# Kernel optimization log

Measured on AMD Instinct MI355X. Metric: run time of the kernel, lower is better.

Reference implementation:

```python
import jax, jax.numpy as jnp
import numpy as np
import math

B, T, D = 2, 2048, 1024
H, HS = 16, 64  # n_heads, head_size; D == H*HS


def setup_inputs() -> dict:
    key = jax.random.key(0)
    k1, k2, k3 = jax.random.split(key, 3)
    x = jax.random.normal(k1, (B, T, D), dtype=jnp.float32)
    w_qkv = jax.random.normal(k2, (D, 3 * D), dtype=jnp.float32) * (1.0 / math.sqrt(D))
    b_qkv = jnp.zeros((3 * D,), dtype=jnp.float32)
    w_out = jax.random.normal(k3, (D, D), dtype=jnp.float32) * (1.0 / math.sqrt(D))
    b_out = jnp.zeros((D,), dtype=jnp.float32)
    return {"x": x, "w_qkv": w_qkv, "b_qkv": b_qkv, "w_out": w_out, "b_out": b_out}


def reference(x, w_qkv, b_qkv, w_out, b_out):
    b, t, d = x.shape
    qkv = x @ w_qkv + b_qkv                       # (B,T,3D)
    q, k, v = jnp.split(qkv, 3, axis=-1)
    # (B,T,D) -> (B,H,T,HS)
    q = q.reshape(b, t, H, HS).transpose(0, 2, 1, 3)
    k = k.reshape(b, t, H, HS).transpose(0, 2, 1, 3)
    v = v.reshape(b, t, H, HS).transpose(0, 2, 1, 3)
    scale = 1.0 / math.sqrt(HS)
    attn = jnp.einsum('bhqd,bhkd->bhqk', q, k) * scale  # (B,H,T,T)
    causal = jnp.tril(jnp.ones((t, t), dtype=bool))
    attn = jnp.where(causal[None, None], attn, -jnp.inf)
    attn = jax.nn.softmax(attn, axis=-1)
    o = jnp.einsum('bhqk,bhkd->bhqd', attn, v)          # (B,H,T,HS)
    o = o.transpose(0, 2, 1, 3).reshape(b, t, d)
    return o @ w_out + b_out
```

## Files before the change

### kernel.cpp

```cpp
#include <hip/hip_runtime.h>
#include <math.h>

#define B_  2
#define T_  2048
#define D_  1024
#define H_  16
#define HS_ 64
#define M_  (B_*T_)

typedef __bf16 bf16x8 __attribute__((ext_vector_type(8)));
typedef float  f32x4  __attribute__((ext_vector_type(4)));
typedef unsigned short u16;

static __device__ __forceinline__ u16 f2bf(float f) {
    __bf16 h = (__bf16)f;
    return *reinterpret_cast<u16*>(&h);
}

static __device__ __forceinline__ void glds16(const u16* g, u16* l) {
    __builtin_amdgcn_global_load_lds(
        (const __attribute__((address_space(1))) void*)g,
        (__attribute__((address_space(3))) void*)l, 16, 0, 0);
}

__global__ __launch_bounds__(256) void prep_kernel(
    const float* __restrict__ x, const float* __restrict__ w_qkv,
    const float* __restrict__ w_out,
    u16* __restrict__ Xb, u16* __restrict__ WqkvT, u16* __restrict__ WoutT)
{
    int bid = blockIdx.x;
    if (bid < 4096) {
        int i = (bid * 256 + threadIdx.x) * 4;
        float4 v = *reinterpret_cast<const float4*>(x + i);
        ushort4 o;
        o.x = f2bf(v.x); o.y = f2bf(v.y); o.z = f2bf(v.z); o.w = f2bf(v.w);
        *reinterpret_cast<ushort4*>(Xb + i) = o;
        return;
    }
    const float* in; u16* out; int C; int c0, r0;
    if (bid < 4096 + 3072) {
        int t = bid - 4096;
        in = w_qkv; out = WqkvT; C = 3 * D_;
        c0 = (t % 96) * 32; r0 = (t / 96) * 32;
    } else {
        int t = bid - 7168;
        in = w_out; out = WoutT; C = D_;
        c0 = (t & 31) * 32; r0 = (t >> 5) * 32;
    }
    __shared__ float tile[32][33];
    int tr = threadIdx.x >> 3, tc4 = (threadIdx.x & 7) * 4;
    float4 v = *reinterpret_cast<const float4*>(in + (size_t)(r0 + tr) * C + c0 + tc4);
    tile[tr][tc4+0] = v.x; tile[tr][tc4+1] = v.y;
    tile[tr][tc4+2] = v.z; tile[tr][tc4+3] = v.w;
    __syncthreads();
    ushort4 o;
    o.x = f2bf(tile[tc4+0][tr]); o.y = f2bf(tile[tc4+1][tr]);
    o.z = f2bf(tile[tc4+2][tr]); o.w = f2bf(tile[tc4+3][tr]);
    *reinterpret_cast<ushort4*>(out + (size_t)(c0 + tr) * D_ + r0 + tc4) = o;
}

template<int MODE, int BM, int BN, int WM, int WN, int NTH>
__global__ __launch_bounds__(NTH, 2) void gemm_bt2(
    const u16* __restrict__ A, const u16* __restrict__ Bt,
    const float* __restrict__ bias,
    float* __restrict__ Cf,
    u16* __restrict__ Qb, u16* __restrict__ Kb, u16* __restrict__ Vt,
    int M, int N, int K)
{
    constexpr int MF  = BM / WM / 16;
    constexpr int NF  = BN / WN / 16;
    constexpr int NLA = BM * 8 / NTH;
    constexpr int NLB = BN * 8 / NTH;

    __shared__ u16 As[2][BM * 64];
    __shared__ u16 Bs[2][BN * 64];

    const int tid  = threadIdx.x;
    const int lane = tid & 63, wave = tid >> 6;
    const int wm = wave / WN, wn = wave % WN;
    const int quad = lane >> 4, lr = lane & 15, x7 = lane & 7;
    const int bm = blockIdx.x, bn = blockIdx.y;

    const u16* Ab = A  + (size_t)(bm * BM) * K;
    const u16* Bb = Bt + (size_t)(bn * BN) * K;

    const u16* srcA[NLA]; int dA[NLA];
    const u16* srcB[NLB]; int dB[NLB];
    #pragma unroll
    for (int j = 0; j < NLA; ++j) {
        int ci = j * NTH + tid, r = ci >> 3, c = (ci & 7) ^ (r & 7);
        srcA[j] = Ab + (size_t)r * K + c * 8;
        dA[j] = ci * 8;
    }
    #pragma unroll
    for (int j = 0; j < NLB; ++j) {
        int ci = j * NTH + tid, r = ci >> 3, c = (ci & 7) ^ (r & 7);
        srcB[j] = Bb + (size_t)r * K + c * 8;
        dB[j] = ci * 8;
    }

    const int eA0 = (wm*(BM/WM) + lr)*64 + ((quad    ) ^ x7)*8;
    const int eA1 = (wm*(BM/WM) + lr)*64 + ((quad | 4) ^ x7)*8;
    const int eB0 = (wn*(BN/WN) + lr)*64 + ((quad    ) ^ x7)*8;
    const int eB1 = (wn*(BN/WN) + lr)*64 + ((quad | 4) ^ x7)*8;

    f32x4 acc[MF][NF] = {};
    const int NT = K >> 6;

    #pragma unroll
    for (int j = 0; j < NLA; ++j) glds16(srcA[j], &As[0][dA[j]]);
    #pragma unroll
    for (int j = 0; j < NLB; ++j) glds16(srcB[j], &Bs[0][dB[j]]);
    #pragma unroll
    for (int j = 0; j < NLA; ++j) glds16(srcA[j] + 64, &As[1][dA[j]]);
    #pragma unroll
    for (int j = 0; j < NLB; ++j) glds16(srcB[j] + 64, &Bs[1][dB[j]]);
    asm volatile("s_waitcnt vmcnt(8)" ::: "memory");
    __builtin_amdgcn_s_barrier();

    for (int t = 0; t < NT; ++t) {
        const u16* Ac = As[t & 1];
        const u16* Bc = Bs[t & 1];
        bf16x8 a[MF], b[NF];

        #pragma unroll
        for (int i = 0; i < MF; ++i)
            a[i] = *reinterpret_cast<const bf16x8*>(Ac + eA0 + i*1024);
        #pragma unroll
        for (int j = 0; j < NF; ++j)
            b[j] = *reinterpret_cast<const bf16x8*>(Bc + eB0 + j*1024);
        __builtin_amdgcn_s_setprio(1);
        #pragma unroll
        for (int i = 0; i < MF; ++i)
            #pragma unroll
            for (int j = 0; j < NF; ++j)
                acc[i][j] = __builtin_amdgcn_mfma_f32_16x16x32_bf16(a[i], b[j], acc[i][j], 0, 0, 0);
        __builtin_amdgcn_s_setprio(0);

        #pragma unroll
        for (int i = 0; i < MF; ++i)
            a[i] = *reinterpret_cast<const bf16x8*>(Ac + eA1 + i*1024);
        #pragma unroll
        for (int j = 0; j < NF; ++j)
            b[j] = *reinterpret_cast<const bf16x8*>(Bc + eB1 + j*1024);
        asm volatile("s_waitcnt lgkmcnt(0)" ::: "memory");
        __builtin_amdgcn_s_barrier();

        if (t + 2 < NT) {
            const int k0 = (t + 2) << 6;
            u16* Ad = As[t & 1]; u16* Bd = Bs[t & 1];
            #pragma unroll
            for (int j = 0; j < NLA; ++j) glds16(srcA[j] + k0, Ad + dA[j]);
            #pragma unroll
            for (int j = 0; j < NLB; ++j) glds16(srcB[j] + k0, Bd + dB[j]);
        }

        __builtin_amdgcn_s_setprio(1);
        #pragma unroll
        for (int i = 0; i < MF; ++i)
            #pragma unroll
            for (int j = 0; j < NF; ++j)
                acc[i][j] = __builtin_amdgcn_mfma_f32_16x16x32_bf16(a[i], b[j], acc[i][j], 0, 0, 0);
        __builtin_amdgcn_s_setprio(0);

        if (t + 2 < NT) { asm volatile("s_waitcnt vmcnt(8)" ::: "memory"); }
        else           { asm volatile("s_waitcnt vmcnt(0)" ::: "memory"); }
        __builtin_amdgcn_s_barrier();
    }

    #pragma unroll
    for (int i = 0; i < MF; ++i) {
        int m0 = bm*BM + wm*(BM/WM) + i*16 + quad*4;
        #pragma unroll
        for (int j = 0; j < NF; ++j) {
            int ncol = bn*BN + wn*(BN/WN) + j*16 + lr;
            float bv = bias[ncol];
            float v4[4];
            #pragma unroll
            for (int r = 0; r < 4; ++r) v4[r] = acc[i][j][r] + bv;
            if (MODE == 1) {
                #pragma unroll
                for (int r = 0; r < 4; ++r)
                    Cf[(size_t)(m0 + r) * N + ncol] = v4[r];
            } else {
                int bb = m0 >> 11, t0 = m0 & (T_ - 1);
                int s = ncol >> 10, rem = ncol & 1023;
                int h = rem >> 6, d = rem & 63;
                int bh = bb * H_ + h;
                if (s == 0) {
                    #pragma unroll
                    for (int r = 0; r < 4; ++r)
                        Qb[((size_t)bh*T_ + t0 + r)*HS_ + d] = f2bf(v4[r] * 0.1803368801111244f);
                } else if (s == 1) {
                    #pragma unroll
                    for (int r = 0; r < 4; ++r)
                        Kb[((size_t)bh*T_ + t0 + r)*HS_ + d] = f2bf(v4[r]);
                } else {
                    ushort4 o;
                    o.x = f2bf(v4[0]); o.y = f2bf(v4[1]);
                    o.z = f2bf(v4[2]); o.w = f2bf(v4[3]);
                    *reinterpret_cast<ushort4*>(&Vt[((size_t)bh*HS_ + d)*T_ + t0]) = o;
                }
            }
        }
    }
}

__global__ __launch_bounds__(256) void attn_kernel(
    const u16* __restrict__ Qb, const u16* __restrict__ Kb,
    const u16* __restrict__ Vt, u16* __restrict__ Ob)
{
    __shared__ u16 Ks[64 * 64];
    __shared__ u16 Vs[64 * 64];
    __shared__ u16 Ps[4][16 * 64];

    int tid  = threadIdx.x;
    int lane = tid & 63, wave = tid >> 6;
    int quad = lane >> 4, lr = lane & 15;

    int lin = blockIdx.x;
    int bh  = (lin & 7) + 8 * ((lin >> 3) & 3);
    int idx = lin >> 5;
    int qt  = idx < 16 ? idx : 47 - idx;
    int qw  = qt * 64 + wave * 16;

    const u16* Qp = Qb + ((size_t)bh * T_ + qw) * HS_;
    bf16x8 qf[2];
    #pragma unroll
    for (int h2 = 0; h2 < 2; ++h2)
        qf[h2] = *reinterpret_cast<const bf16x8*>(Qp + lr*HS_ + h2*32 + quad*8);

    f32x4 Oa[4] = {};
    float lrow[4] = {0.f, 0.f, 0.f, 0.f};

    int e      = quad ^ (lr & 7);
    int rb0    = (lr * 8 + e) * 8;
    int rb1    = (lr * 8 + (e ^ 4)) * 8;
    int offw[4][4];
    #pragma unroll
    for (int nt = 0; nt < 4; ++nt)
        #pragma unroll
        for (int r = 0; r < 4; ++r) {
            int prow = quad*4 + r;
            offw[nt][r] = (prow*8 + ((nt*2 + (lr >> 3)) ^ (prow & 7)))*8 + (lr & 7);
        }
    u16* Psw = Ps[wave];

    int srow = tid >> 3;
    int scol = ((tid & 7) ^ (srow & 7)) * 8;
    const u16* kp0 = Kb + ((size_t)bh*T_ + srow     )*HS_ + scol;
    const u16* kp1 = Kb + ((size_t)bh*T_ + srow + 32)*HS_ + scol;
    const u16* vp0 = Vt + ((size_t)bh*HS_ + srow     )*T_ + scol;
    const u16* vp1 = Vt + ((size_t)bh*HS_ + srow + 32)*T_ + scol;

    bf16x8 kpre0 = *reinterpret_cast<const bf16x8*>(kp0);
    bf16x8 kpre1 = *reinterpret_cast<const bf16x8*>(kp1);
    bf16x8 vpre0 = *reinterpret_cast<const bf16x8*>(vp0);
    bf16x8 vpre1 = *reinterpret_cast<const bf16x8*>(vp1);

    for (int jt = 0; jt <= qt; ++jt) {
        __syncthreads();
        reinterpret_cast<bf16x8*>(Ks)[tid]       = kpre0;
        reinterpret_cast<bf16x8*>(Ks)[tid + 256] = kpre1;
        reinterpret_cast<bf16x8*>(Vs)[tid]       = vpre0;
        reinterpret_cast<bf16x8*>(Vs)[tid + 256] = vpre1;
        if (jt < qt) {
            kp0 += 64*HS_; kp1 += 64*HS_; vp0 += 64; vp1 += 64;
            kpre0 = *reinterpret_cast<const bf16x8*>(kp0);
            kpre1 = *reinterpret_cast<const bf16x8*>(kp1);
            vpre0 = *reinterpret_cast<const bf16x8*>(vp0);
            vpre1 = *reinterpret_cast<const bf16x8*>(vp1);
        }
        __syncthreads();

        f32x4 Sa[4] = {};
        #pragma unroll
        for (int nt = 0; nt < 4; ++nt) {
            bf16x8 bk0 = *reinterpret_cast<const bf16x8*>(Ks + rb0 + nt*1024);
            bf16x8 bk1 = *reinterpret_cast<const bf16x8*>(Ks + rb1 + nt*1024);
            Sa[nt] = __builtin_amdgcn_mfma_f32_16x16x32_bf16(qf[0], bk0, Sa[nt], 0, 0, 0);
            Sa[nt] = __builtin_amdgcn_mfma_f32_16x16x32_bf16(qf[1], bk1, Sa[nt], 0, 0, 0);
        }

        if (jt == qt) {
            int kb = jt * 64;
            #pragma unroll
            for (int nt = 0; nt < 4; ++nt)
                #pragma unroll
                for (int r = 0; r < 4; ++r) {
                    int kg = kb + nt*16 + lr;
                    int qg = qw + quad*4 + r;
                    if (kg > qg) Sa[nt][r] = -INFINITY;
                }
        }

        #pragma unroll
        for (int nt = 0; nt < 4; ++nt)
            #pragma unroll
            for (int r = 0; r < 4; ++r) {
                float pv = __builtin_amdgcn_exp2f(Sa[nt][r]);
                lrow[r] += pv;
                Psw[offw[nt][r]] = f2bf(pv);
            }

        #pragma unroll
        for (int kk = 0; kk < 2; ++kk) {
            int rb = kk ? rb1 : rb0;
            bf16x8 pa = *reinterpret_cast<const bf16x8*>(Psw + rb);
            #pragma unroll
            for (int nt = 0; nt < 4; ++nt) {
                bf16x8 vb = *reinterpret_cast<const bf16x8*>(Vs + rb + nt*1024);
                Oa[nt] = __builtin_amdgcn_mfma_f32_16x16x32_bf16(pa, vb, Oa[nt], 0, 0, 0);
            }
        }
    }

    int b = bh >> 4, h = bh & 15;
    #pragma unroll
    for (int r = 0; r < 4; ++r) {
        float s = lrow[r];
        #pragma unroll
        for (int off = 8; off >= 1; off >>= 1)
            s += __shfl_xor(s, off, 64);
        float inv = 1.f / s;
        int qg = qw + quad*4 + r;
        #pragma unroll
        for (int nt = 0; nt < 4; ++nt) {
            int d = nt*16 + lr;
            Ob[((size_t)b*T_ + qg)*D_ + h*HS_ + d] = f2bf(Oa[nt][r] * inv);
        }
    }
}

extern "C" void kernel_launch(void* const* d_in, const int* in_sizes, int n_in,
                              void* d_out, int out_size, void* d_ws, size_t ws_size,
                              hipStream_t stream) {
    (void)in_sizes; (void)n_in; (void)out_size; (void)ws_size;
    const float* x     = (const float*)d_in[0];
    const float* w_qkv = (const float*)d_in[1];
    const float* b_qkv = (const float*)d_in[2];
    const float* w_out = (const float*)d_in[3];
    const float* b_out = (const float*)d_in[4];
    float* out = (float*)d_out;

    char* ws = (char*)d_ws;
    u16* Xb    = (u16*)ws; ws += (size_t)M_ * D_ * 2;
    u16* WqkvT = (u16*)ws; ws += (size_t)3 * D_ * D_ * 2;
    u16* WoutT = (u16*)ws; ws += (size_t)D_ * D_ * 2;
    u16* Qb    = (u16*)ws; ws += (size_t)M_ * D_ * 2;
    u16* Kb    = (u16*)ws; ws += (size_t)M_ * D_ * 2;
    u16* Vt    = (u16*)ws; ws += (size_t)M_ * D_ * 2;
    u16* Ob    = (u16*)ws; ws += (size_t)M_ * D_ * 2;

    prep_kernel<<<8192, 256, 0, stream>>>(x, w_qkv, w_out, Xb, WqkvT, WoutT);
    gemm_bt2<0, 256, 256, 2, 4, 512><<<dim3(M_/256, 3*D_/256), 512, 0, stream>>>(
        Xb, WqkvT, b_qkv, nullptr, Qb, Kb, Vt, M_, 3*D_, D_);
    attn_kernel<<<1024, 256, 0, stream>>>(Qb, Kb, Vt, Ob);
    gemm_bt2<1, 128, 128, 2, 2, 256><<<dim3(M_/128, D_/128), 256, 0, stream>>>(
        Ob, WoutT, b_out, out, nullptr, nullptr, nullptr, M_, D_, D_);
}
```

Before: 175.7 us.

## Add dedicated QKV GEMM kernel with split-K-half staging and interleaved MFMA pipeline

Replaces the templated GEMM for the QKV projection with a specialized kernel that splits each 64-wide K tile into two 32-wide halves held in separate XOR-swizzled LDS buffers. Global-to-LDS loads for the next tile are issued in four pieces between MFMA quarter-blocks, with barriers and waitcnt placed to overlap memory with compute. The aim is to hide load latency and cut LDS bank conflicts. The cost is many more barriers per iteration and more complex synchronization. The generic GEMM is reduced to the output-projection mode only.

```diff
diff --git a/kernel.cpp b/kernel.cpp
--- a/kernel.cpp
+++ b/kernel.cpp
@@ -59,12 +59,149 @@
     *reinterpret_cast<ushort4*>(out + (size_t)(c0 + tr) * D_ + r0 + tc4) = o;
 }
 
+__global__ __launch_bounds__(512, 2) void gemm_qkv(
+    const u16* __restrict__ A, const u16* __restrict__ Bt,
+    const float* __restrict__ bias,
+    u16* __restrict__ Qb, u16* __restrict__ Kb, u16* __restrict__ Vt)
+{
+    constexpr int K  = D_;
+    constexpr int NT = K / 64;
+
+    __shared__ u16 LDS[2][2][2][8192];
+
+    const int tid  = threadIdx.x;
+    const int lane = tid & 63, wave = tid >> 6;
+    const int wm = wave >> 2, wn = wave & 3;
+    const int quad = lane >> 4, lr = lane & 15;
+    const int bm = blockIdx.x, bn = blockIdx.y;
+
+    const u16* Ab = A  + (size_t)(bm * 256) * K;
+    const u16* Bb = Bt + (size_t)(bn * 256) * K;
+
+    const int r0 = tid >> 2;
+    const int c0 = (tid & 3) ^ ((tid >> 3) & 3);
+    const u16* sA0 = Ab + (size_t)r0 * K + c0 * 8;
+    const u16* sA1 = sA0 + (size_t)128 * K;
+    const u16* sB0 = Bb + (size_t)r0 * K + c0 * 8;
+    const u16* sB1 = sB0 + (size_t)128 * K;
+    const int d0 = tid * 8, d1 = (tid + 512) * 8;
+
+    const int swz = (lr >> 1) & 3;
+    const int eA = ((wm*128 + lr) * 4 + (quad ^ swz)) * 8;
+    const int eB = ((wn*64  + lr) * 4 + (quad ^ swz)) * 8;
+
+    f32x4 acc[8][4] = {};
+
+#define STG(mat, kh, tt) do { \
+        u16* _d = &LDS[(tt) & 1][mat][kh][0]; \
+        const int _ko = (tt) * 64 + (kh) * 32; \
+        glds16(((mat) ? sB0 : sA0) + _ko, _d + d0); \
+        glds16(((mat) ? sB1 : sA1) + _ko, _d + d1); \
+    } while (0)
+
+#define MFMA_QUAD(mh) do { \
+        __builtin_amdgcn_s_setprio(1); \
+        _Pragma("unroll") \
+        for (int i_ = 0; i_ < 4; ++i_) \
+            _Pragma("unroll") \
+            for (int j_ = 0; j_ < 4; ++j_) \
+                acc[(mh)*4 + i_][j_] = __builtin_amdgcn_mfma_f32_16x16x32_bf16( \
+                    a[i_], b[j_], acc[(mh)*4 + i_][j_], 0, 0, 0); \
+        __builtin_amdgcn_s_setprio(0); \
+    } while (0)
+
+    STG(0,0,0); STG(1,0,0); STG(0,1,0); STG(1,1,0);
+    asm volatile("s_waitcnt vmcnt(4)" ::: "memory");
+    __builtin_amdgcn_s_barrier();
+
+    for (int t = 0; t < NT; ++t) {
+        const int cb = t & 1;
+        const bool last = (t == NT - 1);
+        const u16* Ar0 = &LDS[cb][0][0][0];
+        const u16* Ar1 = &LDS[cb][0][1][0];
+        const u16* Br0 = &LDS[cb][1][0][0];
+        const u16* Br1 = &LDS[cb][1][1][0];
+        bf16x8 a[4], b[4];
+
+        #pragma unroll
+        for (int i = 0; i < 4; ++i) a[i] = *reinterpret_cast<const bf16x8*>(Ar0 + eA + i*512);
+        #pragma unroll
+        for (int j = 0; j < 4; ++j) b[j] = *reinterpret_cast<const bf16x8*>(Br0 + eB + j*512);
+        if (!last) STG(0,0,t+1);
+        __builtin_amdgcn_s_barrier();
+        asm volatile("s_waitcnt lgkmcnt(0)" ::: "memory");
+        MFMA_QUAD(0);
+        __builtin_amdgcn_s_barrier();
+
+        #pragma unroll
+        for (int i = 0; i < 4; ++i) a[i] = *reinterpret_cast<const bf16x8*>(Ar0 + eA + (i+4)*512);
+        if (!last) STG(1,0,t+1);
+        __builtin_amdgcn_s_barrier();
+        asm volatile("s_waitcnt lgkmcnt(0)" ::: "memory");
+        MFMA_QUAD(1);
+        if (!last) { asm volatile("s_waitcnt vmcnt(4)" ::: "memory"); }
+        else       { asm volatile("s_waitcnt vmcnt(0)" ::: "memory"); }
+        __builtin_amdgcn_s_barrier();
+
+        #pragma unroll
+        for (int i = 0; i < 4; ++i) a[i] = *reinterpret_cast<const bf16x8*>(Ar1 + eA + i*512);
+        #pragma unroll
+        for (int j = 0; j < 4; ++j) b[j] = *reinterpret_cast<const bf16x8*>(Br1 + eB + j*512);
+        if (!last) STG(0,1,t+1);
+        __builtin_amdgcn_s_barrier();
+        asm volatile("s_waitcnt lgkmcnt(0)" ::: "memory");
+        MFMA_QUAD(0);
+        __builtin_amdgcn_s_barrier();
+
+        #pragma unroll
+        for (int i = 0; i < 4; ++i) a[i] = *reinterpret_cast<const bf16x8*>(Ar1 + eA + (i+4)*512);
+        if (!last) STG(1,1,t+1);
+        __builtin_amdgcn_s_barrier();
+        asm volatile("s_waitcnt lgkmcnt(0)" ::: "memory");
+        MFMA_QUAD(1);
+        asm volatile("s_waitcnt vmcnt(4)" ::: "memory");
+        __builtin_amdgcn_s_barrier();
+    }
+#undef STG
+#undef MFMA_QUAD
+
+    #pragma unroll
+    for (int i = 0; i < 8; ++i) {
+        int m0 = bm*256 + wm*128 + i*16 + quad*4;
+        #pragma unroll
+        for (int j = 0; j < 4; ++j) {
+            int ncol = bn*256 + wn*64 + j*16 + lr;
+            float bv = bias[ncol];
+            float v4[4];
+            #pragma unroll
+            for (int r = 0; r < 4; ++r) v4[r] = acc[i][j][r] + bv;
+            int bb = m0 >> 11, t0 = m0 & (T_ - 1);
+            int s = ncol >> 10, rem = ncol & 1023;
+            int h = rem >> 6, d = rem & 63;
+            int bh = bb * H_ + h;
+            if (s == 0) {
+                #pragma unroll
+                for (int r = 0; r < 4; ++r)
+                    Qb[((size_t)bh*T_ + t0 + r)*HS_ + d] = f2bf(v4[r] * 0.1803368801111244f);
+            } else if (s == 1) {
+                #pragma unroll
+                for (int r = 0; r < 4; ++r)
+                    Kb[((size_t)bh*T_ + t0 + r)*HS_ + d] = f2bf(v4[r]);
+            } else {
+                ushort4 o;
+                o.x = f2bf(v4[0]); o.y = f2bf(v4[1]);
+                o.z = f2bf(v4[2]); o.w = f2bf(v4[3]);
+                *reinterpret_cast<ushort4*>(&Vt[((size_t)bh*HS_ + d)*T_ + t0]) = o;
+            }
+        }
+    }
+}
+
 template<int MODE, int BM, int BN, int WM, int WN, int NTH>
 __global__ __launch_bounds__(NTH, 2) void gemm_bt2(
     const u16* __restrict__ A, const u16* __restrict__ Bt,
     const float* __restrict__ bias,
     float* __restrict__ Cf,
-    u16* __restrict__ Qb, u16* __restrict__ Kb, u16* __restrict__ Vt,
     int M, int N, int K)
 {
     constexpr int MF  = BM / WM / 16;
@@ -175,33 +312,9 @@
         for (int j = 0; j < NF; ++j) {
             int ncol = bn*BN + wn*(BN/WN) + j*16 + lr;
             float bv = bias[ncol];
-            float v4[4];
-            #pragma unroll
-            for (int r = 0; r < 4; ++r) v4[r] = acc[i][j][r] + bv;
-            if (MODE == 1) {
-                #pragma unroll
-                for (int r = 0; r < 4; ++r)
-                    Cf[(size_t)(m0 + r) * N + ncol] = v4[r];
-            } else {
-                int bb = m0 >> 11, t0 = m0 & (T_ - 1);
-                int s = ncol >> 10, rem = ncol & 1023;
-                int h = rem >> 6, d = rem & 63;
-                int bh = bb * H_ + h;
-                if (s == 0) {
-                    #pragma unroll
-                    for (int r = 0; r < 4; ++r)
-                        Qb[((size_t)bh*T_ + t0 + r)*HS_ + d] = f2bf(v4[r] * 0.1803368801111244f);
-                } else if (s == 1) {
-                    #pragma unroll
-                    for (int r = 0; r < 4; ++r)
-                        Kb[((size_t)bh*T_ + t0 + r)*HS_ + d] = f2bf(v4[r]);
-                } else {
-                    ushort4 o;
-                    o.x = f2bf(v4[0]); o.y = f2bf(v4[1]);
-                    o.z = f2bf(v4[2]); o.w = f2bf(v4[3]);
-                    *reinterpret_cast<ushort4*>(&Vt[((size_t)bh*HS_ + d)*T_ + t0]) = o;
-                }
-            }
+            #pragma unroll
+            for (int r = 0; r < 4; ++r)
+                Cf[(size_t)(m0 + r) * N + ncol] = acc[i][j][r] + bv;
         }
     }
 }
@@ -353,9 +466,9 @@
     u16* Ob    = (u16*)ws; ws += (size_t)M_ * D_ * 2;
 
     prep_kernel<<<8192, 256, 0, stream>>>(x, w_qkv, w_out, Xb, WqkvT, WoutT);
-    gemm_bt2<0, 256, 256, 2, 4, 512><<<dim3(M_/256, 3*D_/256), 512, 0, stream>>>(
-        Xb, WqkvT, b_qkv, nullptr, Qb, Kb, Vt, M_, 3*D_, D_);
+    gemm_qkv<<<dim3(M_/256, 3*D_/256), 512, 0, stream>>>(
+        Xb, WqkvT, b_qkv, Qb, Kb, Vt);
     attn_kernel<<<1024, 256, 0, stream>>>(Qb, Kb, Vt, Ob);
     gemm_bt2<1, 128, 128, 2, 2, 256><<<dim3(M_/128, D_/128), 256, 0, stream>>>(
-        Ob, WoutT, b_out, out, nullptr, nullptr, nullptr, M_, D_, D_);
-}
+        Ob, WoutT, b_out, out, M_, D_, D_);
+}
```

Result: no change. 174.1 us (-0.9%).
